# Kernel optimization log

Measured on AMD Instinct MI355X. Metric: run time of the kernel, lower is better.

Reference implementation:

```python
import jax, jax.numpy as jnp
import numpy as np

D_MODEL = 2048
SSM_RANK = 8            # ultra_config.ar_ssm_max_rank = 8
FFN_RANK = D_MODEL // 64  # = 32, UltraLowRankFFN default rank
EPS = 1e-5


def setup_inputs() -> dict:
    key = jax.random.key(0)
    ks = jax.random.split(key, 10)
    d, r, rf = D_MODEL, SSM_RANK, FFN_RANK
    sc = 0.01  # xavier-ish small gain init mirroring gain=0.01
    return {
        "x": jax.random.normal(ks[0], (4, 4096, d), dtype=jnp.float32),
        # shared LayerNorm (used for both pre-norms)
        "ln_gamma": jnp.ones((d,), jnp.float32),
        "ln_beta": jnp.zeros((d,), jnp.float32),
        # AR-SSM (adaptive-rank semiseparable): input proj, per-rank decay, output proj, skip D
        "W_in": jax.random.normal(ks[1], (d, r), jnp.float32) * (1.0 / np.sqrt(d)),
        "b_in": jnp.zeros((r,), jnp.float32),
        "decay_logit": jax.random.normal(ks[2], (r,), jnp.float32),
        "W_out": jax.random.normal(ks[3], (r, d), jnp.float32) * (1.0 / np.sqrt(r)),
        "b_out": jnp.zeros((d,), jnp.float32),
        "D_skip": jax.random.normal(ks[4], (d,), jnp.float32) * 0.1,
        # Ultra low-rank FFN
        "W_down": jax.random.normal(ks[5], (d, rf), jnp.float32) * sc,
        "b_down": jnp.zeros((rf,), jnp.float32),
        "W_up": jax.random.normal(ks[6], (rf, d), jnp.float32) * sc,
        "b_up": jnp.zeros((d,), jnp.float32),
    }


def _layernorm(x, gamma, beta):
    mu = jnp.mean(x, axis=-1, keepdims=True)
    var = jnp.var(x, axis=-1, keepdims=True)
    return (x - mu) * jax.lax.rsqrt(var + EPS) * gamma + beta


def _ssm_scan(u, decay):
    # h_t = decay * h_{t-1} + u_t ; u: [B,S,r], decay: [r]
    a = jnp.broadcast_to(decay, u.shape)

    def combine(e1, e2):
        a1, b1 = e1
        a2, b2 = e2
        return a1 * a2, a2 * b1 + b2

    _, h = jax.lax.associative_scan(combine, (a, u), axis=1)
    return h  # [B,S,r]


def reference(x, ln_gamma, ln_beta, W_in, b_in, decay_logit, W_out, b_out,
              D_skip, W_down, b_down, W_up, b_up):
    # --- AR-SSM sub-block (pre-norm) ---
    xn = _layernorm(x, ln_gamma, ln_beta)
    u = jnp.einsum("bsd,dr->bsr", xn, W_in) + b_in          # low-rank input proj
    decay = jax.nn.sigmoid(decay_logit)                       # per-rank decay in (0,1)
    h = _ssm_scan(u, decay)                                   # semiseparable scan
    x_ar = jnp.einsum("bsr,rd->bsd", h, W_out) + b_out + xn * D_skip
    x = x + x_ar
    # --- Ultra low-rank FFN sub-block (same shared norm) ---
    xn2 = _layernorm(x, ln_gamma, ln_beta)
    hf = jax.nn.relu(jnp.einsum("bsd,dr->bsr", xn2, W_down) + b_down)
    x_ffn = jnp.einsum("bsr,rd->bsd", hf, W_up) + b_up
    return x + x_ffn
```

## Files before the change

kernel.cpp:

```cpp
#include <hip/hip_runtime.h>
#include <cstdint>
#include <cstddef>

#define D_MODEL 2048
#define EPSF 1e-5f

#define WS_UT    0
#define WS_MU1   131072
#define WS_RSIG1 147456
#define WS_WDT   163840
#define WS_WINF  229376
#define WS_C     245760
#define WS_D     245792
#define WS_CIN   245824
#define WS_DIN   245832

__device__ __forceinline__ float4 ld4(const float* __restrict__ p) {
    return *(const float4*)p;
}
__device__ __forceinline__ void st4(float* __restrict__ p, float4 v) {
    *(float4*)p = v;
}
__device__ __forceinline__ int bitrev6(int l) {
    return ((l & 1) << 5) | ((l & 2) << 3) | ((l & 4) << 1) |
           ((l & 8) >> 1) | ((l & 16) >> 3) | ((l & 32) >> 5);
}
__device__ __forceinline__ int bitrev4(int l) {
    return ((l & 1) << 3) | ((l & 2) << 1) | ((l & 4) >> 1) | ((l & 8) >> 3);
}

__global__ __launch_bounds__(64) void k0_prep(
    const float* __restrict__ Win, const float* __restrict__ b_in,
    const float* __restrict__ Wd, const float* __restrict__ gamma,
    const float* __restrict__ beta, const float* __restrict__ bd,
    float* __restrict__ ws)
{
    const int t = threadIdx.x;
    const int blk = blockIdx.x;
    if (blk < 8) {
        __shared__ float tile[64 * 33];
        const int gblk = blk;
        for (int cc = 0; cc < 4; ++cc) {
            const int ibase = gblk * 256 + cc * 64;
#pragma unroll
            for (int m = 0; m < 32; ++m) {
                const int e = m * 64 + t;
                const int il = e >> 5, j = e & 31;
                tile[il * 33 + j] = Wd[(size_t)ibase * 32 + e];
            }
            __syncthreads();
#pragma unroll
            for (int j = 0; j < 32; ++j) {
                const int i = ibase + t;
                ws[WS_WDT + (size_t)j * 2048 + i] = gamma[i] * tile[t * 33 + j];
            }
            __syncthreads();
        }
    } else if (blk == 8) {
        const int j = t & 31, h = t >> 5;
        float cacc = 0.f, dacc = 0.f;
        for (int k = 0; k < 1024; ++k) {
            const int i = h * 1024 + k;
            const float w = Wd[(size_t)i * 32 + j];
            cacc = fmaf(gamma[i], w, cacc);
            dacc = fmaf(beta[i], w, dacc);
        }
        cacc += __shfl_xor(cacc, 32, 64);
        dacc += __shfl_xor(dacc, 32, 64);
        if (t < 32) {
            ws[WS_C + j] = cacc;
            ws[WS_D + j] = dacc + bd[j];
        }
    } else {
        float cj[8], dj[8];
#pragma unroll
        for (int j = 0; j < 8; ++j) { cj[j] = 0.f; dj[j] = 0.f; }
        for (int k = 0; k < 32; ++k) {
            const int i = k * 64 + t;
            const float g = gamma[i], b = beta[i];
            float4 w0 = ld4(Win + (size_t)i * 8);
            float4 w1 = ld4(Win + (size_t)i * 8 + 4);
            st4(ws + WS_WINF + (size_t)i * 8,
                make_float4(g * w0.x, g * w0.y, g * w0.z, g * w0.w));
            st4(ws + WS_WINF + (size_t)i * 8 + 4,
                make_float4(g * w1.x, g * w1.y, g * w1.z, g * w1.w));
            cj[0] = fmaf(g, w0.x, cj[0]); cj[1] = fmaf(g, w0.y, cj[1]);
            cj[2] = fmaf(g, w0.z, cj[2]); cj[3] = fmaf(g, w0.w, cj[3]);
            cj[4] = fmaf(g, w1.x, cj[4]); cj[5] = fmaf(g, w1.y, cj[5]);
            cj[6] = fmaf(g, w1.z, cj[6]); cj[7] = fmaf(g, w1.w, cj[7]);
            dj[0] = fmaf(b, w0.x, dj[0]); dj[1] = fmaf(b, w0.y, dj[1]);
            dj[2] = fmaf(b, w0.z, dj[2]); dj[3] = fmaf(b, w0.w, dj[3]);
            dj[4] = fmaf(b, w1.x, dj[4]); dj[5] = fmaf(b, w1.y, dj[5]);
            dj[6] = fmaf(b, w1.z, dj[6]); dj[7] = fmaf(b, w1.w, dj[7]);
        }
#pragma unroll
        for (int off = 1; off < 64; off <<= 1) {
#pragma unroll
            for (int j = 0; j < 8; ++j) {
                cj[j] += __shfl_xor(cj[j], off, 64);
                dj[j] += __shfl_xor(dj[j], off, 64);
            }
        }
        if (t == 0) {
#pragma unroll
            for (int j = 0; j < 8; ++j) {
                ws[WS_CIN + j] = cj[j];
                ws[WS_DIN + j] = dj[j] + b_in[j];
            }
        }
    }
}

__global__ __launch_bounds__(256) void k1_ln_u(
    const float* __restrict__ x, float* __restrict__ ws)
{
    __shared__ float red[8][4][12];
    const int t = threadIdx.x;
    const int wv = t >> 6, lane = t & 63;
    const int row0 = blockIdx.x * 8;
    const int i0 = t * 8;

    float winf[64];
#pragma unroll
    for (int q = 0; q < 16; ++q) {
        float4 v = ld4(ws + WS_WINF + (size_t)i0 * 8 + q * 4);
        winf[q*4+0] = v.x; winf[q*4+1] = v.y; winf[q*4+2] = v.z; winf[q*4+3] = v.w;
    }
    float xv[8][8];
#pragma unroll
    for (int rr = 0; rr < 8; ++rr) {
        const float* xr = x + (size_t)(row0 + rr) * D_MODEL + i0;
        float4 a = ld4(xr), b = ld4(xr + 4);
        xv[rr][0]=a.x; xv[rr][1]=a.y; xv[rr][2]=a.z; xv[rr][3]=a.w;
        xv[rr][4]=b.x; xv[rr][5]=b.y; xv[rr][6]=b.z; xv[rr][7]=b.w;
    }
#pragma unroll
    for (int rr = 0; rr < 8; ++rr) {
        float vals[16];
#pragma unroll
        for (int v = 0; v < 16; ++v) vals[v] = 0.f;
#pragma unroll
        for (int i = 0; i < 8; ++i) {
            const float xi = xv[rr][i];
            vals[0] += xi;
            vals[1] = fmaf(xi, xi, vals[1]);
#pragma unroll
            for (int j = 0; j < 8; ++j)
                vals[2+j] = fmaf(xi, winf[i*8 + j], vals[2+j]);
        }
        int count = 16;
#pragma unroll
        for (int step = 1; step <= 32; step <<= 1) {
            if (count > 1) {
                const int half = count >> 1;
                const bool up = (lane & step) != 0;
#pragma unroll
                for (int k = 0; k < 8; ++k) {
                    if (k < half) {
                        float send = vals[up ? k : k + half];
                        float keep = vals[up ? k + half : k];
                        vals[k] = keep + __shfl_xor(send, step, 64);
                    }
                }
                count = half;
            } else {
                vals[0] += __shfl_xor(vals[0], step, 64);
            }
        }
        if (lane < 16) {
            const int v = bitrev4(lane);
            if (v < 10) red[rr][wv][v] = vals[0];
        }
    }
    __syncthreads();
    if (t < 64) {
        const int row = t >> 3, j = t & 7;
        float s_ = 0.f, q_ = 0.f, uraw = 0.f;
#pragma unroll
        for (int w = 0; w < 4; ++w) {
            s_   += red[row][w][0];
            q_   += red[row][w][1];
            uraw += red[row][w][2 + j];
        }
        const float mu = s_ * (1.f / D_MODEL);
        const float var = q_ * (1.f / D_MODEL) - mu * mu;
        const float rs = rsqrtf(var + EPSF);
        const float u = fmaf(rs, fmaf(-mu, ws[WS_CIN + j], uraw), ws[WS_DIN + j]);
        const int grow = row0 + row;
        const int bb = grow >> 12, s0 = grow & 4095;
        ws[WS_UT + ((size_t)bb * 8 + j) * 4096 + s0] = u;
        if (j == 0) {
            ws[WS_MU1 + grow] = mu;
            ws[WS_RSIG1 + grow] = rs;
        }
    }
}

__global__ __launch_bounds__(64) void k2_scan(
    const float* __restrict__ logit, float* __restrict__ ws)
{
    const int t = threadIdx.x;
    const int blk = blockIdx.x;
    const int b = blk >> 3, r = blk & 7;
    const float a = 1.f / (1.f + expf(-logit[r]));
    float* u = ws + WS_UT + ((size_t)b * 8 + r) * 4096 + t * 64;
    float v[64];
#pragma unroll
    for (int q = 0; q < 16; ++q) {
        float4 w = ld4(u + q * 4);
        v[q*4]=w.x; v[q*4+1]=w.y; v[q*4+2]=w.z; v[q*4+3]=w.w;
    }
    float c = 0.f;
#pragma unroll
    for (int k = 0; k < 64; ++k) { c = fmaf(a, c, v[k]); v[k] = c; }
    float A = a;
#pragma unroll
    for (int i = 0; i < 6; ++i) A *= A;
    float Bv = c, Aa = A;
#pragma unroll
    for (int off = 1; off < 64; off <<= 1) {
        float Ap = __shfl_up(Aa, off, 64);
        float Bp = __shfl_up(Bv, off, 64);
        if (t >= off) { Bv = fmaf(Aa, Bp, Bv); Aa *= Ap; }
    }
    float P = __shfl_up(Bv, 1, 64);
    if (t == 0) P = 0.f;
    float f = a * P;
#pragma unroll
    for (int k = 0; k < 64; ++k) { v[k] += f; f *= a; }
#pragma unroll
    for (int q = 0; q < 16; ++q)
        st4(u + q * 4, make_float4(v[q*4], v[q*4+1], v[q*4+2], v[q*4+3]));
}

__global__ __launch_bounds__(256) void k3_fused(
    const float* __restrict__ x, const float* __restrict__ gamma,
    const float* __restrict__ beta, const float* __restrict__ Wout,
    const float* __restrict__ b_out, const float* __restrict__ Dsk,
    const float* __restrict__ Wu, const float* __restrict__ bu,
    float* __restrict__ out, float* __restrict__ ws)
{
    __shared__ float Y[8 * 2048];
    __shared__ float shf[8 * 32];
    __shared__ float smu2[8], srs2[8];
    const int t = threadIdx.x;
    const int blk = blockIdx.x;
    const int r = t >> 5, l = t & 31;
    const int row = blk * 8 + r;
    const int bb = row >> 12, s = row & 4095;
    const float mu1 = ws[WS_MU1 + row], rs1 = ws[WS_RSIG1 + row];
    float h[8];
#pragma unroll
    for (int j = 0; j < 8; ++j)
        h[j] = ws[WS_UT + ((size_t)bb * 8 + j) * 4096 + s];
    const float* xr = x + (size_t)row * D_MODEL;
    float sum = 0.f, ssq = 0.f;
#pragma unroll 2
    for (int k = 0; k < 16; ++k) {
        const int i = k * 128 + l * 4;
        float4 xvv = ld4(xr + i);
        float4 gv = ld4(gamma + i), bv = ld4(beta + i);
        float4 bo = ld4(b_out + i), dk = ld4(Dsk + i);
        float4 acc = bo;
#pragma unroll
        for (int j = 0; j < 8; ++j) {
            float4 w = ld4(Wout + (size_t)j * D_MODEL + i);
            acc.x = fmaf(h[j], w.x, acc.x);
            acc.y = fmaf(h[j], w.y, acc.y);
            acc.z = fmaf(h[j], w.z, acc.z);
            acc.w = fmaf(h[j], w.w, acc.w);
        }
        float4 xn;
        xn.x = fmaf((xvv.x - mu1) * rs1, gv.x, bv.x);
        xn.y = fmaf((xvv.y - mu1) * rs1, gv.y, bv.y);
        xn.z = fmaf((xvv.z - mu1) * rs1, gv.z, bv.z);
        xn.w = fmaf((xvv.w - mu1) * rs1, gv.w, bv.w);
        acc.x = fmaf(xn.x, dk.x, acc.x);
        acc.y = fmaf(xn.y, dk.y, acc.y);
        acc.z = fmaf(xn.z, dk.z, acc.z);
        acc.w = fmaf(xn.w, dk.w, acc.w);
        float4 x2;
        x2.x = xvv.x + acc.x; x2.y = xvv.y + acc.y;
        x2.z = xvv.z + acc.z; x2.w = xvv.w + acc.w;
        st4(&Y[r * 2048 + i], x2);
        sum += x2.x + x2.y + x2.z + x2.w;
        ssq = fmaf(x2.x, x2.x, ssq); ssq = fmaf(x2.y, x2.y, ssq);
        ssq = fmaf(x2.z, x2.z, ssq); ssq = fmaf(x2.w, x2.w, ssq);
    }
#pragma unroll
    for (int off = 1; off < 32; off <<= 1) {
        sum += __shfl_xor(sum, off, 64);
        ssq += __shfl_xor(ssq, off, 64);
    }
    if (l == 0) {
        const float mu2 = sum * (1.f / D_MODEL);
        const float var = ssq * (1.f / D_MODEL) - mu2 * mu2;
        smu2[r] = mu2;
        srs2[r] = rsqrtf(var + EPSF);
    }
    __syncthreads();

    const int wvb = t >> 6, lane = t & 63;
    const int jb = wvb * 8;
    float p[64];
#pragma unroll
    for (int v = 0; v < 64; ++v) p[v] = 0.f;
#pragma unroll 1
    for (int q = 0; q < 8; ++q) {
        const int ip = q * 256 + lane * 4;
        float4 yv[8];
#pragma unroll
        for (int rr = 0; rr < 8; ++rr) yv[rr] = ld4(&Y[rr * 2048 + ip]);
#pragma unroll
        for (int jj = 0; jj < 8; ++jj) {
            float4 w = ld4(ws + WS_WDT + (size_t)(jb + jj) * 2048 + ip);
#pragma unroll
            for (int rr = 0; rr < 8; ++rr) {
                p[rr*8+jj] = fmaf(yv[rr].x, w.x, p[rr*8+jj]);
                p[rr*8+jj] = fmaf(yv[rr].y, w.y, p[rr*8+jj]);
                p[rr*8+jj] = fmaf(yv[rr].z, w.z, p[rr*8+jj]);
                p[rr*8+jj] = fmaf(yv[rr].w, w.w, p[rr*8+jj]);
            }
        }
    }
    {
        int count = 64;
#pragma unroll
        for (int step = 1; step <= 32; step <<= 1) {
            const int half = count >> 1;
            const bool up = (lane & step) != 0;
#pragma unroll
            for (int k = 0; k < 32; ++k) {
                if (k < half) {
                    float send = p[up ? k : k + half];
                    float keep = p[up ? k + half : k];
                    p[k] = keep + __shfl_xor(send, step, 64);
                }
            }
            count = half;
        }
    }
    {
        const int v = bitrev6(lane);
        const int r_ = v >> 3, j_ = v & 7;
        const float mu2r = smu2[r_], rs2r = srs2[r_];
        const float cj = ws[WS_C + jb + j_], dj = ws[WS_D + jb + j_];
        shf[r_ * 32 + jb + j_] =
            fmaxf(0.f, fmaf(rs2r, fmaf(-mu2r, cj, p[0]), dj));
    }
    __syncthreads();

    const int c0 = t * 4;
    float4 a0[8], a1[8];
    const float4 bu0 = ld4(bu + c0), bu1 = ld4(bu + 1024 + c0);
#pragma unroll
    for (int rr = 0; rr < 8; ++rr) {
        float4 y0 = ld4(&Y[rr * 2048 + c0]);
        float4 y1 = ld4(&Y[rr * 2048 + 1024 + c0]);
        a0[rr] = make_float4(y0.x + bu0.x, y0.y + bu0.y, y0.z + bu0.z, y0.w + bu0.w);
        a1[rr] = make_float4(y1.x + bu1.x, y1.y + bu1.y, y1.z + bu1.z, y1.w + bu1.w);
    }
#pragma unroll 1
    for (int jc = 0; jc < 8; ++jc) {
        float hv[8][4];
#pragma unroll
        for (int rr = 0; rr < 8; ++rr) {
            float4 hq = ld4(&shf[rr * 32 + jc * 4]);
            hv[rr][0] = hq.x; hv[rr][1] = hq.y; hv[rr][2] = hq.z; hv[rr][3] = hq.w;
        }
#pragma unroll
        for (int jj = 0; jj < 4; ++jj) {
            const int j = jc * 4 + jj;
            const float4 w0 = ld4(Wu + (size_t)j * D_MODEL + c0);
            const float4 w1 = ld4(Wu + (size_t)j * D_MODEL + 1024 + c0);
#pragma unroll
            for (int rr = 0; rr < 8; ++rr) {
                const float hval = hv[rr][jj];
                a0[rr].x = fmaf(hval, w0.x, a0[rr].x);
                a0[rr].y = fmaf(hval, w0.y, a0[rr].y);
                a0[rr].z = fmaf(hval, w0.z, a0[rr].z);
                a0[rr].w = fmaf(hval, w0.w, a0[rr].w);
                a1[rr].x = fmaf(hval, w1.x, a1[rr].x);
                a1[rr].y = fmaf(hval, w1.y, a1[rr].y);
                a1[rr].z = fmaf(hval, w1.z, a1[rr].z);
                a1[rr].w = fmaf(hval, w1.w, a1[rr].w);
            }
        }
    }
#pragma unroll
    for (int rr = 0; rr < 8; ++rr) {
        float* orow = out + (size_t)(blk * 8 + rr) * D_MODEL;
        st4(orow + c0, a0[rr]);
        st4(orow + 1024 + c0, a1[rr]);
    }
}

extern "C" void kernel_launch(void* const* d_in, const int* in_sizes, int n_in,
                              void* d_out, int out_size, void* d_ws, size_t ws_size,
                              hipStream_t stream) {
    const float* x      = (const float*)d_in[0];
    const float* gamma  = (const float*)d_in[1];
    const float* beta   = (const float*)d_in[2];
    const float* Win    = (const float*)d_in[3];
    const float* b_in   = (const float*)d_in[4];
    const float* logit  = (const float*)d_in[5];
    const float* Wout   = (const float*)d_in[6];
    const float* b_out  = (const float*)d_in[7];
    const float* Dsk    = (const float*)d_in[8];
    const float* Wd     = (const float*)d_in[9];
    const float* bd     = (const float*)d_in[10];
    const float* Wu     = (const float*)d_in[11];
    const float* bu     = (const float*)d_in[12];
    float* out = (float*)d_out;
    float* ws  = (float*)d_ws;

    hipLaunchKernelGGL(k0_prep, dim3(10),   dim3(64),  0, stream,
                       Win, b_in, Wd, gamma, beta, bd, ws);
    hipLaunchKernelGGL(k1_ln_u, dim3(2048), dim3(256), 0, stream, x, ws);
    hipLaunchKernelGGL(k2_scan, dim3(32),   dim3(64),  0, stream, logit, ws);
    hipLaunchKernelGGL(k3_fused, dim3(2048), dim3(256), 0, stream,
                       x, gamma, beta, Wout, b_out, Dsk, Wu, bu, out, ws);
}
```

Measured before the change: 496.9 us.

## Restructure k3 first phase by column and software-pipeline weight loads

```diff
diff --git a/kernel.cpp b/kernel.cpp
--- a/kernel.cpp
+++ b/kernel.cpp
@@ -111,7 +111,7 @@
     }
 }
 
-__global__ __launch_bounds__(256) void k1_ln_u(
+__global__ __launch_bounds__(256, 4) void k1_ln_u(
     const float* __restrict__ x, float* __restrict__ ws)
 {
     __shared__ float red[8][4][12];
@@ -126,22 +126,24 @@
         float4 v = ld4(ws + WS_WINF + (size_t)i0 * 8 + q * 4);
         winf[q*4+0] = v.x; winf[q*4+1] = v.y; winf[q*4+2] = v.z; winf[q*4+3] = v.w;
     }
-    float xv[8][8];
-#pragma unroll
+    float4 xa = ld4(x + (size_t)row0 * D_MODEL + i0);
+    float4 xb = ld4(x + (size_t)row0 * D_MODEL + i0 + 4);
+#pragma unroll 1
     for (int rr = 0; rr < 8; ++rr) {
-        const float* xr = x + (size_t)(row0 + rr) * D_MODEL + i0;
-        float4 a = ld4(xr), b = ld4(xr + 4);
-        xv[rr][0]=a.x; xv[rr][1]=a.y; xv[rr][2]=a.z; xv[rr][3]=a.w;
-        xv[rr][4]=b.x; xv[rr][5]=b.y; xv[rr][6]=b.z; xv[rr][7]=b.w;
-    }
-#pragma unroll
-    for (int rr = 0; rr < 8; ++rr) {
+        float xc[8];
+        xc[0]=xa.x; xc[1]=xa.y; xc[2]=xa.z; xc[3]=xa.w;
+        xc[4]=xb.x; xc[5]=xb.y; xc[6]=xb.z; xc[7]=xb.w;
+        if (rr < 7) {
+            const float* xr = x + (size_t)(row0 + rr + 1) * D_MODEL + i0;
+            xa = ld4(xr);
+            xb = ld4(xr + 4);
+        }
         float vals[16];
 #pragma unroll
         for (int v = 0; v < 16; ++v) vals[v] = 0.f;
 #pragma unroll
         for (int i = 0; i < 8; ++i) {
-            const float xi = xv[rr][i];
+            const float xi = xc[i];
             vals[0] += xi;
             vals[1] = fmaf(xi, xi, vals[1]);
 #pragma unroll
@@ -233,7 +235,7 @@
         st4(u + q * 4, make_float4(v[q*4], v[q*4+1], v[q*4+2], v[q*4+3]));
 }
 
-__global__ __launch_bounds__(256) void k3_fused(
+__global__ __launch_bounds__(256, 2) void k3_fused(
     const float* __restrict__ x, const float* __restrict__ gamma,
     const float* __restrict__ beta, const float* __restrict__ Wout,
     const float* __restrict__ b_out, const float* __restrict__ Dsk,
@@ -241,87 +243,147 @@
     float* __restrict__ out, float* __restrict__ ws)
 {
     __shared__ float Y[8 * 2048];
+    __shared__ float sh_h[8][8];
+    __shared__ float smu1[8], srs1[8];
+    __shared__ float smu2[8], srs2[8];
+    __shared__ float red2[16][4];
     __shared__ float shf[8 * 32];
-    __shared__ float smu2[8], srs2[8];
     const int t = threadIdx.x;
     const int blk = blockIdx.x;
-    const int r = t >> 5, l = t & 31;
-    const int row = blk * 8 + r;
-    const int bb = row >> 12, s = row & 4095;
-    const float mu1 = ws[WS_MU1 + row], rs1 = ws[WS_RSIG1 + row];
-    float h[8];
-#pragma unroll
-    for (int j = 0; j < 8; ++j)
-        h[j] = ws[WS_UT + ((size_t)bb * 8 + j) * 4096 + s];
-    const float* xr = x + (size_t)row * D_MODEL;
-    float sum = 0.f, ssq = 0.f;
-#pragma unroll 2
-    for (int k = 0; k < 16; ++k) {
-        const int i = k * 128 + l * 4;
-        float4 xvv = ld4(xr + i);
-        float4 gv = ld4(gamma + i), bv = ld4(beta + i);
-        float4 bo = ld4(b_out + i), dk = ld4(Dsk + i);
-        float4 acc = bo;
-#pragma unroll
-        for (int j = 0; j < 8; ++j) {
-            float4 w = ld4(Wout + (size_t)j * D_MODEL + i);
-            acc.x = fmaf(h[j], w.x, acc.x);
-            acc.y = fmaf(h[j], w.y, acc.y);
-            acc.z = fmaf(h[j], w.z, acc.z);
-            acc.w = fmaf(h[j], w.w, acc.w);
-        }
-        float4 xn;
-        xn.x = fmaf((xvv.x - mu1) * rs1, gv.x, bv.x);
-        xn.y = fmaf((xvv.y - mu1) * rs1, gv.y, bv.y);
-        xn.z = fmaf((xvv.z - mu1) * rs1, gv.z, bv.z);
-        xn.w = fmaf((xvv.w - mu1) * rs1, gv.w, bv.w);
-        acc.x = fmaf(xn.x, dk.x, acc.x);
-        acc.y = fmaf(xn.y, dk.y, acc.y);
-        acc.z = fmaf(xn.z, dk.z, acc.z);
-        acc.w = fmaf(xn.w, dk.w, acc.w);
-        float4 x2;
-        x2.x = xvv.x + acc.x; x2.y = xvv.y + acc.y;
-        x2.z = xvv.z + acc.z; x2.w = xvv.w + acc.w;
-        st4(&Y[r * 2048 + i], x2);
-        sum += x2.x + x2.y + x2.z + x2.w;
-        ssq = fmaf(x2.x, x2.x, ssq); ssq = fmaf(x2.y, x2.y, ssq);
-        ssq = fmaf(x2.z, x2.z, ssq); ssq = fmaf(x2.w, x2.w, ssq);
-    }
-#pragma unroll
-    for (int off = 1; off < 32; off <<= 1) {
-        sum += __shfl_xor(sum, off, 64);
-        ssq += __shfl_xor(ssq, off, 64);
-    }
-    if (l == 0) {
-        const float mu2 = sum * (1.f / D_MODEL);
-        const float var = ssq * (1.f / D_MODEL) - mu2 * mu2;
-        smu2[r] = mu2;
-        srs2[r] = rsqrtf(var + EPSF);
+    const int row0 = blk * 8;
+    const int wv = t >> 6, lane = t & 63;
+
+    if (t < 64) {
+        const int r_ = t >> 3, j_ = t & 7;
+        const int grow = row0 + r_;
+        const int bb = grow >> 12, s = grow & 4095;
+        sh_h[r_][j_] = ws[WS_UT + ((size_t)bb * 8 + j_) * 4096 + s];
+        if (j_ == 0) {
+            smu1[r_] = ws[WS_MU1 + grow];
+            srs1[r_] = ws[WS_RSIG1 + grow];
+        }
     }
     __syncthreads();
 
-    const int wvb = t >> 6, lane = t & 63;
-    const int jb = wvb * 8;
+    float hreg[64];
+#pragma unroll
+    for (int r = 0; r < 8; ++r) {
+        float4 h0 = ld4(&sh_h[r][0]);
+        float4 h1 = ld4(&sh_h[r][4]);
+        hreg[r*8+0]=h0.x; hreg[r*8+1]=h0.y; hreg[r*8+2]=h0.z; hreg[r*8+3]=h0.w;
+        hreg[r*8+4]=h1.x; hreg[r*8+5]=h1.y; hreg[r*8+6]=h1.z; hreg[r*8+7]=h1.w;
+    }
+
+    float sum[8], ssq[8];
+#pragma unroll
+    for (int r = 0; r < 8; ++r) { sum[r] = 0.f; ssq[r] = 0.f; }
+
+#pragma unroll 1
+    for (int pass = 0; pass < 2; ++pass) {
+        const int c = pass * 1024 + t * 4;
+        const float4 g = ld4(gamma + c), bt = ld4(beta + c);
+        const float4 bo = ld4(b_out + c), dk = ld4(Dsk + c);
+        float4 wo[8];
+#pragma unroll
+        for (int j = 0; j < 8; ++j) wo[j] = ld4(Wout + (size_t)j * D_MODEL + c);
+#pragma unroll
+        for (int r = 0; r < 8; ++r) {
+            const float4 xv = ld4(x + (size_t)(row0 + r) * D_MODEL + c);
+            const float mu1 = smu1[r], rs1 = srs1[r];
+            float4 acc = bo;
+#pragma unroll
+            for (int j = 0; j < 8; ++j) {
+                const float hj = hreg[r*8 + j];
+                acc.x = fmaf(hj, wo[j].x, acc.x);
+                acc.y = fmaf(hj, wo[j].y, acc.y);
+                acc.z = fmaf(hj, wo[j].z, acc.z);
+                acc.w = fmaf(hj, wo[j].w, acc.w);
+            }
+            float4 xn;
+            xn.x = fmaf((xv.x - mu1) * rs1, g.x, bt.x);
+            xn.y = fmaf((xv.y - mu1) * rs1, g.y, bt.y);
+            xn.z = fmaf((xv.z - mu1) * rs1, g.z, bt.z);
+            xn.w = fmaf((xv.w - mu1) * rs1, g.w, bt.w);
+            acc.x = fmaf(xn.x, dk.x, acc.x);
+            acc.y = fmaf(xn.y, dk.y, acc.y);
+            acc.z = fmaf(xn.z, dk.z, acc.z);
+            acc.w = fmaf(xn.w, dk.w, acc.w);
+            float4 x2;
+            x2.x = xv.x + acc.x; x2.y = xv.y + acc.y;
+            x2.z = xv.z + acc.z; x2.w = xv.w + acc.w;
+            st4(&Y[r * 2048 + c], x2);
+            sum[r] += x2.x + x2.y + x2.z + x2.w;
+            ssq[r] = fmaf(x2.x, x2.x, ssq[r]); ssq[r] = fmaf(x2.y, x2.y, ssq[r]);
+            ssq[r] = fmaf(x2.z, x2.z, ssq[r]); ssq[r] = fmaf(x2.w, x2.w, ssq[r]);
+        }
+    }
+    {
+        float vals[16];
+#pragma unroll
+        for (int r = 0; r < 8; ++r) { vals[r] = sum[r]; vals[8+r] = ssq[r]; }
+        int count = 16;
+#pragma unroll
+        for (int step = 1; step <= 32; step <<= 1) {
+            if (count > 1) {
+                const int half = count >> 1;
+                const bool up = (lane & step) != 0;
+#pragma unroll
+                for (int k = 0; k < 8; ++k) {
+                    if (k < half) {
+                        float send = vals[up ? k : k + half];
+                        float keep = vals[up ? k + half : k];
+                        vals[k] = keep + __shfl_xor(send, step, 64);
+                    }
+                }
+                count = half;
+            } else {
+                vals[0] += __shfl_xor(vals[0], step, 64);
+            }
+        }
+        if (lane < 16) red2[bitrev4(lane)][wv] = vals[0];
+    }
+    __syncthreads();
+    if (t < 8) {
+        float s_ = red2[t][0] + red2[t][1] + red2[t][2] + red2[t][3];
+        float q_ = red2[8+t][0] + red2[8+t][1] + red2[8+t][2] + red2[8+t][3];
+        const float mu2 = s_ * (1.f / D_MODEL);
+        const float var = q_ * (1.f / D_MODEL) - mu2 * mu2;
+        smu2[t] = mu2;
+        srs2[t] = rsqrtf(var + EPSF);
+    }
+    __syncthreads();
+
+    const int jb = wv * 8;
     float p[64];
 #pragma unroll
     for (int v = 0; v < 64; ++v) p[v] = 0.f;
+    float4 wb[8], wbn[8];
+#pragma unroll
+    for (int jj = 0; jj < 8; ++jj)
+        wb[jj] = ld4(ws + WS_WDT + (size_t)(jb + jj) * 2048 + lane * 4);
 #pragma unroll 1
     for (int q = 0; q < 8; ++q) {
         const int ip = q * 256 + lane * 4;
+        if (q < 7) {
+#pragma unroll
+            for (int jj = 0; jj < 8; ++jj)
+                wbn[jj] = ld4(ws + WS_WDT + (size_t)(jb + jj) * 2048 + ip + 256);
+        }
         float4 yv[8];
 #pragma unroll
         for (int rr = 0; rr < 8; ++rr) yv[rr] = ld4(&Y[rr * 2048 + ip]);
 #pragma unroll
         for (int jj = 0; jj < 8; ++jj) {
-            float4 w = ld4(ws + WS_WDT + (size_t)(jb + jj) * 2048 + ip);
 #pragma unroll
             for (int rr = 0; rr < 8; ++rr) {
-                p[rr*8+jj] = fmaf(yv[rr].x, w.x, p[rr*8+jj]);
-                p[rr*8+jj] = fmaf(yv[rr].y, w.y, p[rr*8+jj]);
-                p[rr*8+jj] = fmaf(yv[rr].z, w.z, p[rr*8+jj]);
-                p[rr*8+jj] = fmaf(yv[rr].w, w.w, p[rr*8+jj]);
-            }
-        }
+                p[rr*8+jj] = fmaf(yv[rr].x, wb[jj].x, p[rr*8+jj]);
+                p[rr*8+jj] = fmaf(yv[rr].y, wb[jj].y, p[rr*8+jj]);
+                p[rr*8+jj] = fmaf(yv[rr].z, wb[jj].z, p[rr*8+jj]);
+                p[rr*8+jj] = fmaf(yv[rr].w, wb[jj].w, p[rr*8+jj]);
+            }
+        }
+#pragma unroll
+        for (int jj = 0; jj < 8; ++jj) wb[jj] = wbn[jj];
     }
     {
         int count = 64;
@@ -360,36 +422,46 @@
         a0[rr] = make_float4(y0.x + bu0.x, y0.y + bu0.y, y0.z + bu0.z, y0.w + bu0.w);
         a1[rr] = make_float4(y1.x + bu1.x, y1.y + bu1.y, y1.z + bu1.z, y1.w + bu1.w);
     }
+    float4 w0[4], w1[4], w0n[4], w1n[4];
+#pragma unroll
+    for (int jj = 0; jj < 4; ++jj) {
+        w0[jj] = ld4(Wu + (size_t)jj * D_MODEL + c0);
+        w1[jj] = ld4(Wu + (size_t)jj * D_MODEL + 1024 + c0);
+    }
 #pragma unroll 1
     for (int jc = 0; jc < 8; ++jc) {
-        float hv[8][4];
-#pragma unroll
-        for (int rr = 0; rr < 8; ++rr) {
-            float4 hq = ld4(&shf[rr * 32 + jc * 4]);
-            hv[rr][0] = hq.x; hv[rr][1] = hq.y; hv[rr][2] = hq.z; hv[rr][3] = hq.w;
-        }
+        if (jc < 7) {
+#pragma unroll
+            for (int jj = 0; jj < 4; ++jj) {
+                w0n[jj] = ld4(Wu + (size_t)((jc+1)*4 + jj) * D_MODEL + c0);
+                w1n[jj] = ld4(Wu + (size_t)((jc+1)*4 + jj) * D_MODEL + 1024 + c0);
+            }
+        }
+        float4 hq[8];
+#pragma unroll
+        for (int rr = 0; rr < 8; ++rr) hq[rr] = ld4(&shf[rr * 32 + jc * 4]);
 #pragma unroll
         for (int jj = 0; jj < 4; ++jj) {
-            const int j = jc * 4 + jj;
-            const float4 w0 = ld4(Wu + (size_t)j * D_MODEL + c0);
-            const float4 w1 = ld4(Wu + (size_t)j * D_MODEL + 1024 + c0);
 #pragma unroll
             for (int rr = 0; rr < 8; ++rr) {
-                const float hval = hv[rr][jj];
-                a0[rr].x = fmaf(hval, w0.x, a0[rr].x);
-                a0[rr].y = fmaf(hval, w0.y, a0[rr].y);
-                a0[rr].z = fmaf(hval, w0.z, a0[rr].z);
-                a0[rr].w = fmaf(hval, w0.w, a0[rr].w);
-                a1[rr].x = fmaf(hval, w1.x, a1[rr].x);
-                a1[rr].y = fmaf(hval, w1.y, a1[rr].y);
-                a1[rr].z = fmaf(hval, w1.z, a1[rr].z);
-                a1[rr].w = fmaf(hval, w1.w, a1[rr].w);
-            }
-        }
+                const float hval = (jj == 0) ? hq[rr].x : (jj == 1) ? hq[rr].y
+                                 : (jj == 2) ? hq[rr].z : hq[rr].w;
+                a0[rr].x = fmaf(hval, w0[jj].x, a0[rr].x);
+                a0[rr].y = fmaf(hval, w0[jj].y, a0[rr].y);
+                a0[rr].z = fmaf(hval, w0[jj].z, a0[rr].z);
+                a0[rr].w = fmaf(hval, w0[jj].w, a0[rr].w);
+                a1[rr].x = fmaf(hval, w1[jj].x, a1[rr].x);
+                a1[rr].y = fmaf(hval, w1[jj].y, a1[rr].y);
+                a1[rr].z = fmaf(hval, w1[jj].z, a1[rr].z);
+                a1[rr].w = fmaf(hval, w1[jj].w, a1[rr].w);
+            }
+        }
+#pragma unroll
+        for (int jj = 0; jj < 4; ++jj) { w0[jj] = w0n[jj]; w1[jj] = w1n[jj]; }
     }
 #pragma unroll
     for (int rr = 0; rr < 8; ++rr) {
-        float* orow = out + (size_t)(blk * 8 + rr) * D_MODEL;
+        float* orow = out + (size_t)(row0 + rr) * D_MODEL;
         st4(orow + c0, a0[rr]);
         st4(orow + 1024 + c0, a1[rr]);
     }
```

After: 502.0 us. Within noise of the previous version (+1.0%).
